# Kernel tuning notes

Measured on AMD Instinct MI355X. Metric: run time of the kernel, lower is better.

## Reference

```python
import jax, jax.numpy as jnp
import numpy as np

TAU = 2.0  # LIF membrane time constant (tau=2.0)
V_TH = 1.0  # spiking threshold (spikingjelly default)

@jax.custom_vjp
def spike(v):
    # Heaviside spike at v >= 0 (input is v - V_TH)
    return (v >= 0.0).astype(v.dtype)

def _spike_fwd(v):
    return spike(v), v

def _spike_bwd(v, g):
    # ATan surrogate gradient (spikingjelly default, alpha=2):
    # d/dv = alpha / (2 * (1 + (pi/2 * alpha * v)^2)) = 1 / (1 + (pi*v)^2)
    return (g / (1.0 + (jnp.pi * v) ** 2),)

spike.defvjp(_spike_fwd, _spike_bwd)

def lif_linear(x, w):
    """SpikLinearLayer: Linear (no bias) then multi-step LIF over leading T axis.
    x: [T, B, N, Din], w: [Dout, Din] -> spikes [T, B, N, Dout]
    LIF: v <- v + (y - v)/tau ; s = H(v - vth) ; hard reset v <- v*(1-s)
    """
    y = jnp.einsum('tbnd,ed->tbne', x, w)
    def step(v, yt):
        v = v + (yt - v) / TAU
        s = spike(v - V_TH)
        return v * (1.0 - s), s
    _, spikes = jax.lax.scan(step, jnp.zeros_like(y[0]), y)
    return spikes

def setup_inputs() -> dict:
    key = jax.random.key(0)
    k0, k1, k2, k3 = jax.random.split(key, 4)
    T, B, N, D, L = 4, 32, 1024, 256, 2
    x = jax.random.normal(k0, (T, B, N, D), dtype=jnp.float32)
    w_in = jax.random.normal(k1, (2 * D, D), dtype=jnp.float32) * 0.05
    w_hidden = jax.random.normal(k2, (L, 2 * D, 2 * D), dtype=jnp.float32) * 0.05
    w_out = jax.random.normal(k3, (D, 2 * D), dtype=jnp.float32) * 0.05
    return {"x": x, "w_in": w_in, "w_hidden": w_hidden, "w_out": w_out}

def reference(x, w_in, w_hidden, w_out):
    # TemporalBlock.forward
    h = lif_linear(x, w_in)                       # [T,B,N,2D]
    for l in range(w_hidden.shape[0]):
        h = h * (1.0 - lif_linear(h, w_hidden[l]))  # multiplicative spike gate
    return lif_linear(h, w_out)                   # [T,B,N,D]
```

## Files before the change

kernel.cpp:

```cpp
#include <hip/hip_runtime.h>
#include <stdint.h>

typedef __attribute__((ext_vector_type(8))) short short8;
typedef __attribute__((ext_vector_type(4))) float f32x4;

constexpr int T_ = 4;
constexpr int BNTOT = 32768;

__device__ __forceinline__ uint32_t bf1(float f) {
    uint32_t x = __builtin_bit_cast(uint32_t, f);
    return (x + 0x7FFFu + ((x >> 16) & 1u)) >> 16;
}
__device__ __forceinline__ uint32_t pk(float lo, float hi) {
    return bf1(lo) | (bf1(hi) << 16);
}

__device__ __forceinline__ short8 expand8(uint2 r) {
    uint4 o;
    o.x = __builtin_amdgcn_perm(0u, r.x, 0x0C010C00u) * 0x3F80u;
    o.y = __builtin_amdgcn_perm(0u, r.x, 0x0C030C02u) * 0x3F80u;
    o.z = __builtin_amdgcn_perm(0u, r.y, 0x0C010C00u) * 0x3F80u;
    o.w = __builtin_amdgcn_perm(0u, r.y, 0x0C030C02u) * 0x3F80u;
    return __builtin_bit_cast(short8, o);
}

__global__ __launch_bounds__(256)
void cvt_tiled(const float* __restrict__ in, ushort* __restrict__ out) {
    const int g  = blockIdx.x * 256 + threadIdx.x;
    const int kg = g & 31;
    const int r  = (g >> 5) & 15;
    const int bt = g >> 9;
    const float* src = in + ((size_t)(bt * 16 + r)) * 256 + kg * 8;
    const float4 a = *(const float4*)src;
    const float4 b = *(const float4*)(src + 4);
    uint4 o;
    o.x = pk(a.x, a.y); o.y = pk(a.z, a.w);
    o.z = pk(b.x, b.y); o.w = pk(b.z, b.w);
    *(uint4*)(out + ((size_t)(bt * 32 + kg)) * 128 + r * 8) = o;
}

template <int MODE, int K, int NOUT>
__global__ __launch_bounds__(256, 2)
void lif_mfma(const void* __restrict__ Av,
              const float* __restrict__ W,
              void* __restrict__ Out)
{
    constexpr int NS = K / 32;
    constexpr int KG = K / 8;
    constexpr int NCOLT = NOUT / 64;
    __shared__ __align__(16) char smem[NS * 4096];

    const int tid = threadIdx.x;
    const int l   = tid & 63;
    const int w   = tid >> 6;

    const int id  = blockIdx.x;
    const int xcd = id & 7;
    const int j_  = id >> 3;
    const int row0 = (xcd * 64 + j_ / NCOLT) * 64;
    const int col0 = (j_ % NCOLT) * 64;

    {
        constexpr int ITERS = 64 * KG / 256;
#pragma unroll
        for (int i = 0; i < ITERS; ++i) {
            const int idx = i * 256 + tid;
            const int c   = idx / KG;
            const int kg  = idx % KG;
            const float* wp = W + (size_t)(col0 + c) * K + kg * 8;
            const float4 f0 = *(const float4*)wp;
            const float4 f1 = *(const float4*)(wp + 4);
            uint4 o;
            o.x = pk(f0.x, f0.y); o.y = pk(f0.z, f0.w);
            o.z = pk(f1.x, f1.y); o.w = pk(f1.z, f1.w);
            *(uint4*)(smem + ((c >> 4) * NS + (kg >> 2)) * 1024 + (c & 15) * 64 +
                      (((kg & 3) ^ ((c >> 1) & 3)) * 16)) = o;
        }
    }
    __syncthreads();

    const char* bbase = smem + (l & 15) * 64 + (((l >> 4) ^ ((l >> 1) & 3)) * 16);
    const int rb = (row0 >> 4) + w;

    f32x4 acc[T_][4];
#pragma unroll
    for (int t = 0; t < T_; ++t)
#pragma unroll
        for (int n = 0; n < 4; ++n) acc[t][n] = (f32x4)0.f;

    size_t aunit[T_];
#pragma unroll
    for (int t = 0; t < T_; ++t)
        aunit[t] = ((size_t)(t * (BNTOT / 16) + rb)) * KG + (l >> 4);

    auto loadAb = [&](int s, short8* a) {
#pragma unroll
        for (int t = 0; t < T_; ++t)
            a[t] = *(const short8*)((const ushort*)Av +
                     (aunit[t] + s * 4) * 128 + (l & 15) * 8);
    };
    auto loadAu = [&](int s, uint2* a) {
#pragma unroll
        for (int t = 0; t < T_; ++t)
            a[t] = *(const uint2*)((const uint8_t*)Av +
                     (aunit[t] + s * 4) * 128 + (l & 15) * 8);
    };
    auto stepB = [&](const short8* a, int s) {
        short8 bfr[4];
#pragma unroll
        for (int n = 0; n < 4; ++n)
            bfr[n] = *(const short8*)(bbase + (n * NS + s) * 1024);
#pragma unroll
        for (int t = 0; t < T_; ++t)
#pragma unroll
            for (int n = 0; n < 4; ++n)
                acc[t][n] = __builtin_amdgcn_mfma_f32_16x16x32_bf16(
                    a[t], bfr[n], acc[t][n], 0, 0, 0);
    };
    auto stepU = [&](const uint2* a, int s) {
        short8 bfr[4];
#pragma unroll
        for (int n = 0; n < 4; ++n)
            bfr[n] = *(const short8*)(bbase + (n * NS + s) * 1024);
#pragma unroll
        for (int t = 0; t < T_; ++t) {
            const short8 af = expand8(a[t]);
#pragma unroll
            for (int n = 0; n < 4; ++n)
                acc[t][n] = __builtin_amdgcn_mfma_f32_16x16x32_bf16(
                    af, bfr[n], acc[t][n], 0, 0, 0);
        }
    };

    if constexpr (MODE == 0) {
        constexpr int DEPTH = 4;
        short8 a[DEPTH][T_];
#pragma unroll
        for (int p = 0; p < DEPTH; ++p) loadAb(p, a[p]);
#pragma unroll
        for (int s = 0; s < NS; ++s) {
            stepB(a[s % DEPTH], s);
            if (s + DEPTH < NS) loadAb(s + DEPTH, a[s % DEPTH]);
        }
    } else {
        constexpr int DEPTH = 6;
        uint2 a[DEPTH][T_];
#pragma unroll
        for (int p = 0; p < DEPTH; ++p) loadAu(p, a[p]);
#pragma unroll
        for (int s = 0; s < NS; ++s) {
            stepU(a[s % DEPTH], s);
            if (s + DEPTH < NS) loadAu(s + DEPTH, a[s % DEPTH]);
        }
    }

    __syncthreads();

    if constexpr (MODE == 2) {
        float* fl = (float*)smem;
        float v[4][4];
#pragma unroll
        for (int n = 0; n < 4; ++n)
#pragma unroll
            for (int j = 0; j < 4; ++j) v[n][j] = 0.f;
#pragma unroll
        for (int t = 0; t < T_; ++t) {
#pragma unroll
            for (int n = 0; n < 4; ++n)
#pragma unroll
                for (int j = 0; j < 4; ++j) {
                    v[n][j] = 0.5f * (v[n][j] + acc[t][n][j]);
                    const bool sp = (v[n][j] >= 1.f);
                    if (sp) v[n][j] = 0.f;
                    fl[(w * 16 + (l >> 4) * 4 + j) * 68 + n * 16 + (l & 15)] =
                        sp ? 1.f : 0.f;
                }
            __syncthreads();
            const int r  = tid >> 2;
            const int cb = (tid & 3) * 16;
            float* op = (float*)Out +
                ((size_t)(t * BNTOT + row0 + r)) * NOUT + col0 + cb;
#pragma unroll
            for (int k = 0; k < 4; ++k)
                *(float4*)(op + k * 4) = *(const float4*)&fl[r * 68 + cb + k * 4];
            __syncthreads();
        }
    } else {
        char* el = smem;
        float v[4][4];
#pragma unroll
        for (int n = 0; n < 4; ++n)
#pragma unroll
            for (int j = 0; j < 4; ++j) v[n][j] = 0.f;
#pragma unroll
        for (int t = 0; t < T_; ++t)
#pragma unroll
            for (int n = 0; n < 4; ++n)
#pragma unroll
                for (int j = 0; j < 4; ++j) {
                    v[n][j] = 0.5f * (v[n][j] + acc[t][n][j]);
                    const bool sp = (v[n][j] >= 1.f);
                    if (sp) v[n][j] = 0.f;
                    el[t * 4096 + w * 1024 + (n * 2 + ((l & 15) >> 3)) * 128 +
                       ((l >> 4) * 4 + j) * 8 + (l & 7)] =
                        (MODE == 0) ? (sp ? 1 : 0) : (sp ? 0 : 0xFF);
                }
        __syncthreads();
        const int lin = tid * 64;
        const int t  = lin >> 12;
        const int w2 = (lin >> 10) & 3;
        const int cg = (lin >> 7) & 7;
        const size_t gb = ((size_t)(t * (BNTOT / 16) + (row0 >> 4) + w2) *
                          (NOUT / 8) + (col0 >> 3) + cg) * 128 + (lin & 127);
#pragma unroll
        for (int k = 0; k < 4; ++k) {
            uint4 m = *(const uint4*)(el + lin + k * 16);
            if constexpr (MODE == 1) {
                const uint4 h = *(const uint4*)((const uint8_t*)Av + gb + k * 16);
                m.x &= h.x; m.y &= h.y; m.z &= h.z; m.w &= h.w;
            }
            *(uint4*)((uint8_t*)Out + gb + k * 16) = m;
        }
    }
}

extern "C" void kernel_launch(void* const* d_in, const int* in_sizes, int n_in,
                              void* d_out, int out_size, void* d_ws, size_t ws_size,
                              hipStream_t stream)
{
    const float* x     = (const float*)d_in[0];
    const float* w_in  = (const float*)d_in[1];
    const float* w_h   = (const float*)d_in[2];
    const float* w_out = (const float*)d_in[3];

    ushort*  xbf = (ushort*)d_out;
    uint8_t* hA  = (uint8_t*)d_ws;
    uint8_t* hB  = hA + (size_t)T_ * BNTOT * 512;
    float*   out = (float*)d_out;

    cvt_tiled<<<16384, 256, 0, stream>>>(x, xbf);

    lif_mfma<0, 256, 512><<<4096, 256, 0, stream>>>(xbf, w_in, hA);
    lif_mfma<1, 512, 512><<<4096, 256, 0, stream>>>(hA, w_h, hB);
    lif_mfma<1, 512, 512><<<4096, 256, 0, stream>>>(hB, w_h + 512 * 512, hA);
    lif_mfma<2, 512, 256><<<2048, 256, 0, stream>>>(hA, w_out, out);
}
```

Measured before the change: 419.4 us.

## Store hidden spike activations as bf16 and use double-buffered A loads

Intermediate activations and gate masks are now stored as 16-bit bf16 values (0x3F80 / 0xFFFF masks) instead of 8-bit bytes. This removes the per-step expand8 byte-to-bf16 conversion in the MFMA loop and unifies all layers on one load path. The deeper 4/6-stage register prefetch is replaced by a two-buffer ping-pong loop, and the LDS staging of output tiles gains an XOR swizzle. In exchange, intermediate global traffic doubles, prefetch depth shrinks, and the second hidden buffer now reuses d_out.

```diff
diff --git a/kernel.cpp b/kernel.cpp
--- a/kernel.cpp
+++ b/kernel.cpp
@@ -13,15 +13,6 @@
 }
 __device__ __forceinline__ uint32_t pk(float lo, float hi) {
     return bf1(lo) | (bf1(hi) << 16);
-}
-
-__device__ __forceinline__ short8 expand8(uint2 r) {
-    uint4 o;
-    o.x = __builtin_amdgcn_perm(0u, r.x, 0x0C010C00u) * 0x3F80u;
-    o.y = __builtin_amdgcn_perm(0u, r.x, 0x0C030C02u) * 0x3F80u;
-    o.z = __builtin_amdgcn_perm(0u, r.y, 0x0C010C00u) * 0x3F80u;
-    o.w = __builtin_amdgcn_perm(0u, r.y, 0x0C030C02u) * 0x3F80u;
-    return __builtin_bit_cast(short8, o);
 }
 
 __global__ __launch_bounds__(256)
@@ -41,7 +32,7 @@
 
 template <int MODE, int K, int NOUT>
 __global__ __launch_bounds__(256, 2)
-void lif_mfma(const void* __restrict__ Av,
+void lif_mfma(const ushort* __restrict__ A,
               const float* __restrict__ W,
               void* __restrict__ Out)
 {
@@ -57,13 +48,12 @@
     const int id  = blockIdx.x;
     const int xcd = id & 7;
     const int j_  = id >> 3;
-    const int row0 = (xcd * 64 + j_ / NCOLT) * 64;
+    const int row0 = (xcd * (BNTOT / 512) + j_ / NCOLT) * 64;
     const int col0 = (j_ % NCOLT) * 64;
 
     {
-        constexpr int ITERS = 64 * KG / 256;
-#pragma unroll
-        for (int i = 0; i < ITERS; ++i) {
+#pragma unroll
+        for (int i = 0; i < 64 * KG / 256; ++i) {
             const int idx = i * 256 + tid;
             const int c   = idx / KG;
             const int kg  = idx % KG;
@@ -96,14 +86,7 @@
     auto loadAb = [&](int s, short8* a) {
 #pragma unroll
         for (int t = 0; t < T_; ++t)
-            a[t] = *(const short8*)((const ushort*)Av +
-                     (aunit[t] + s * 4) * 128 + (l & 15) * 8);
-    };
-    auto loadAu = [&](int s, uint2* a) {
-#pragma unroll
-        for (int t = 0; t < T_; ++t)
-            a[t] = *(const uint2*)((const uint8_t*)Av +
-                     (aunit[t] + s * 4) * 128 + (l & 15) * 8);
+            a[t] = *(const short8*)(A + (aunit[t] + s * 4) * 128 + (l & 15) * 8);
     };
     auto stepB = [&](const short8* a, int s) {
         short8 bfr[4];
@@ -117,40 +100,15 @@
                 acc[t][n] = __builtin_amdgcn_mfma_f32_16x16x32_bf16(
                     a[t], bfr[n], acc[t][n], 0, 0, 0);
     };
-    auto stepU = [&](const uint2* a, int s) {
-        short8 bfr[4];
-#pragma unroll
-        for (int n = 0; n < 4; ++n)
-            bfr[n] = *(const short8*)(bbase + (n * NS + s) * 1024);
-#pragma unroll
-        for (int t = 0; t < T_; ++t) {
-            const short8 af = expand8(a[t]);
-#pragma unroll
-            for (int n = 0; n < 4; ++n)
-                acc[t][n] = __builtin_amdgcn_mfma_f32_16x16x32_bf16(
-                    af, bfr[n], acc[t][n], 0, 0, 0);
-        }
-    };
-
-    if constexpr (MODE == 0) {
-        constexpr int DEPTH = 4;
-        short8 a[DEPTH][T_];
-#pragma unroll
-        for (int p = 0; p < DEPTH; ++p) loadAb(p, a[p]);
-#pragma unroll
-        for (int s = 0; s < NS; ++s) {
-            stepB(a[s % DEPTH], s);
-            if (s + DEPTH < NS) loadAb(s + DEPTH, a[s % DEPTH]);
-        }
-    } else {
-        constexpr int DEPTH = 6;
-        uint2 a[DEPTH][T_];
-#pragma unroll
-        for (int p = 0; p < DEPTH; ++p) loadAu(p, a[p]);
-#pragma unroll
-        for (int s = 0; s < NS; ++s) {
-            stepU(a[s % DEPTH], s);
-            if (s + DEPTH < NS) loadAu(s + DEPTH, a[s % DEPTH]);
+
+    {
+        short8 aA[T_], aB[T_];
+        loadAb(0, aA);
+        for (int s = 0; s < NS; s += 2) {
+            loadAb(s + 1 < NS ? s + 1 : 0, aB);
+            stepB(aA, s);
+            loadAb(s + 2 < NS ? s + 2 : 0, aA);
+            stepB(aB, s + 1);
         }
     }
 
@@ -186,7 +144,7 @@
             __syncthreads();
         }
     } else {
-        char* el = smem;
+        ushort* el = (ushort*)smem;
         float v[4][4];
 #pragma unroll
         for (int n = 0; n < 4; ++n)
@@ -201,25 +159,30 @@
                     v[n][j] = 0.5f * (v[n][j] + acc[t][n][j]);
                     const bool sp = (v[n][j] >= 1.f);
                     if (sp) v[n][j] = 0.f;
-                    el[t * 4096 + w * 1024 + (n * 2 + ((l & 15) >> 3)) * 128 +
-                       ((l >> 4) * 4 + j) * 8 + (l & 7)] =
-                        (MODE == 0) ? (sp ? 1 : 0) : (sp ? 0 : 0xFF);
+                    const int cg = n * 2 + ((l & 15) >> 3);
+                    const int rl = (l >> 4) * 4 + j;
+                    const int pg = rl ^ cg;
+                    el[(t * 4 + w) * 1024 + cg * 128 + pg * 8 + (l & 7)] =
+                        (MODE == 0) ? (sp ? 0x3F80u : 0u)
+                                    : (sp ? 0u : 0xFFFFu);
                 }
         __syncthreads();
         const int lin = tid * 64;
-        const int t  = lin >> 12;
-        const int w2 = (lin >> 10) & 3;
-        const int cg = (lin >> 7) & 7;
+        const int t   = lin >> 12;
+        const int w2  = (lin >> 10) & 3;
+        const int cg  = (lin >> 7) & 7;
+        const int gh  = (lin >> 6) & 1;
         const size_t gb = ((size_t)(t * (BNTOT / 16) + (row0 >> 4) + w2) *
                           (NOUT / 8) + (col0 >> 3) + cg) * 128 + (lin & 127);
 #pragma unroll
-        for (int k = 0; k < 4; ++k) {
-            uint4 m = *(const uint4*)(el + lin + k * 16);
+        for (int k = 0; k < 8; ++k) {
+            const int pk_ = ((gh * 8 + k) ^ cg) & 15;
+            uint4 m = *(const uint4*)(el + (t * 4 + w2) * 1024 + cg * 128 + pk_ * 8);
             if constexpr (MODE == 1) {
-                const uint4 h = *(const uint4*)((const uint8_t*)Av + gb + k * 16);
+                const uint4 h = *(const uint4*)(A + gb + k * 8);
                 m.x &= h.x; m.y &= h.y; m.z &= h.z; m.w &= h.w;
             }
-            *(uint4*)((uint8_t*)Out + gb + k * 16) = m;
+            *(uint4*)((ushort*)Out + gb + k * 8) = m;
         }
     }
 }
@@ -233,10 +196,10 @@
     const float* w_h   = (const float*)d_in[2];
     const float* w_out = (const float*)d_in[3];
 
-    ushort*  xbf = (ushort*)d_out;
-    uint8_t* hA  = (uint8_t*)d_ws;
-    uint8_t* hB  = hA + (size_t)T_ * BNTOT * 512;
-    float*   out = (float*)d_out;
+    ushort* xbf = (ushort*)d_out;
+    ushort* hA  = (ushort*)d_ws;
+    ushort* hB  = (ushort*)d_out;
+    float*  out = (float*)d_out;
 
     cvt_tiled<<<16384, 256, 0, stream>>>(x, xbf);
 
```

Measured after the change: 544.5 us. 1.3x slower.
